# Kernel tuning notes

Measured on AMD Instinct MI355X. Metric: run time of the kernel, lower is better.

The kernel has to match this reference:

```python
import jax, jax.numpy as jnp
import numpy as np

EPS = 1e-15


def gmm_conv(x, edge_index, edge_attr, g, mu, sigma, root_w, bias):
    # PyG GMMConv (separate_gaussians=False, aggr='mean', root_weight=True)
    N = x.shape[0]
    K, D = mu.shape          # kernel_size, pseudo-coord dim
    M = bias.shape[0]        # out channels
    src, dst = edge_index[0], edge_index[1]
    xg = (x @ g).reshape(N, K, M)            # [N, K, M] transformed source feats
    x_j = xg[src]                            # [E, K, M] gather
    diff = edge_attr[:, None, :] - mu[None]  # [E, K, D]
    gauss = jnp.exp(jnp.sum(-0.5 * diff * diff / (EPS + sigma[None] ** 2), axis=-1))  # [E, K]
    msg = jnp.sum(x_j * gauss[:, :, None], axis=1)          # [E, M]
    agg = jax.ops.segment_sum(msg, dst, num_segments=N)     # scatter-sum
    cnt = jax.ops.segment_sum(jnp.ones((msg.shape[0], 1), msg.dtype), dst, num_segments=N)
    out = agg / jnp.maximum(cnt, 1.0)                        # scatter-mean (0 for isolated nodes)
    return out + x @ root_w + bias


def setup_inputs() -> dict:
    key = jax.random.key(0)
    ks = jax.random.split(key, 16)
    N, E, D, K = 100000, 1600000, 8, 1
    F_in, H, F_out = 32, 32, 32
    inp = {
        "edge_index": jax.random.randint(ks[0], (2, E), 0, N, dtype=jnp.int64)
        if jax.config.jax_enable_x64 else jax.random.randint(ks[0], (2, E), 0, N).astype(jnp.int32),
        "edge_weight": jax.random.normal(ks[1], (E, D), dtype=jnp.float32),
        "x": jax.random.normal(ks[2], (N, F_in), dtype=jnp.float32),
        # layer 1 params
        "g1": jax.random.normal(ks[3], (F_in, K * H), dtype=jnp.float32) * (1.0 / np.sqrt(F_in)),
        "mu1": jax.random.normal(ks[4], (K, D), dtype=jnp.float32),
        "sigma1": jnp.ones((K, D), dtype=jnp.float32),
        "root1": jax.random.normal(ks[5], (F_in, H), dtype=jnp.float32) * (1.0 / np.sqrt(F_in)),
        "b1": jnp.zeros((H,), dtype=jnp.float32),
        # layer 2 params
        "g2": jax.random.normal(ks[6], (H, K * F_out), dtype=jnp.float32) * (1.0 / np.sqrt(H)),
        "mu2": jax.random.normal(ks[7], (K, D), dtype=jnp.float32),
        "sigma2": jnp.ones((K, D), dtype=jnp.float32),
        "root2": jax.random.normal(ks[8], (H, F_out), dtype=jnp.float32) * (1.0 / np.sqrt(H)),
        "b2": jnp.zeros((F_out,), dtype=jnp.float32),
    }
    return inp


def reference(edge_index, edge_weight, x, g1, mu1, sigma1, root1, b1, g2, mu2, sigma2, root2, b2):
    h = gmm_conv(x, edge_index, edge_weight, g1, mu1, sigma1, root1, b1)
    out = gmm_conv(h, edge_index, edge_weight, g2, mu2, sigma2, root2, b2)
    return out
```

## Files before the change

### kernel.cpp

```cpp
#include <hip/hip_runtime.h>

#define F 32
#define D 8
#define BKN 512
#define BKSH 9
#define EPT 8
#define CAP 9216

typedef unsigned uv2 __attribute__((ext_vector_type(2)));
typedef float fv2 __attribute__((ext_vector_type(2)));
typedef float fv4 __attribute__((ext_vector_type(4)));

__device__ __forceinline__ unsigned f2bf(float f) {
    unsigned u = __float_as_uint(f);
    return (u + 0x7fffu + ((u >> 16) & 1u)) >> 16;
}
__device__ __forceinline__ float bf2f(unsigned b) {
    return __uint_as_float(b << 16);
}

__global__ void build_kernel(const int* __restrict__ ei, const float* __restrict__ ew,
                             const float* __restrict__ mu1, const float* __restrict__ sg1,
                             const float* __restrict__ mu2, const float* __restrict__ sg2,
                             int* __restrict__ bcur, uv2* __restrict__ bin, int NB, int E,
                             const float* __restrict__ x, const float* __restrict__ g1,
                             const float* __restrict__ root1, const float* __restrict__ b1,
                             unsigned short* __restrict__ xgh, float* __restrict__ xr,
                             int N, int binBlocks) {
    __shared__ int hist[512];
    __shared__ int cbase[512];
    __shared__ float gs[F * F];
    __shared__ float rs[F * F];
    int t = threadIdx.x;

    if ((int)blockIdx.x < binBlocks) {
        float m1v[D], i1[D], m2v[D], i2[D];
#pragma unroll
        for (int d = 0; d < D; ++d) {
            m1v[d] = mu1[d];
            i1[d] = -0.5f / (1e-15f + sg1[d] * sg1[d]);
            m2v[d] = mu2[d];
            i2[d] = -0.5f / (1e-15f + sg2[d] * sg2[d]);
        }
        if (t < NB) hist[t] = 0;
        __syncthreads();
        int e0 = blockIdx.x * (512 * EPT) + t;
        unsigned pks[EPT], gps[EPT];
        int bks[EPT];
#pragma unroll
        for (int k = 0; k < EPT; ++k) {
            int e = e0 + k * 512;
            bks[k] = -1;
            if (e < E) {
                int src = __builtin_nontemporal_load(&ei[e]);
                int dst = __builtin_nontemporal_load(&ei[E + e]);
                bks[k] = dst >> BKSH;
                pks[k] = (unsigned)src | ((unsigned)(dst & (BKN - 1)) << 20);
                const fv4* ew4 = (const fv4*)(ew + (size_t)e * D);
                fv4 w0 = __builtin_nontemporal_load(ew4);
                fv4 w1 = __builtin_nontemporal_load(ew4 + 1);
                float w[D] = {w0.x, w0.y, w0.z, w0.w, w1.x, w1.y, w1.z, w1.w};
                float s1 = 0.f, s2 = 0.f;
#pragma unroll
                for (int d = 0; d < D; ++d) {
                    float d1 = w[d] - m1v[d];
                    s1 += d1 * d1 * i1[d];
                    float d2 = w[d] - m2v[d];
                    s2 += d2 * d2 * i2[d];
                }
                gps[k] = f2bf(expf(s1)) | (f2bf(expf(s2)) << 16);
                atomicAdd(&hist[bks[k]], 1);
            }
        }
        __syncthreads();
        if (t < NB) {
            int c = hist[t];
            cbase[t] = t * CAP + (c ? atomicAdd(&bcur[t], c) : 0);
        }
        __syncthreads();
        if (t < NB) hist[t] = 0;
        __syncthreads();
#pragma unroll
        for (int k = 0; k < EPT; ++k) {
            if (bks[k] >= 0) {
                int pos = cbase[bks[k]] + atomicAdd(&hist[bks[k]], 1);
                if (pos < (bks[k] + 1) * CAP) {
                    uv2 p;
                    p.x = pks[k];
                    p.y = gps[k];
                    bin[pos] = p;
                }
            }
        }
    } else {
        for (int i = t; i < F * F; i += 512) {
            gs[i] = g1[i];
            rs[i] = root1[i];
        }
        __syncthreads();
        int m = t & 31;
        int node = (int)((((size_t)blockIdx.x - binBlocks) * 512 + t) >> 5);
        if (node >= N) return;
        float xv = x[(size_t)node * F + m];
        int base = t & 32;
        float accg = 0.f, accr = 0.f;
#pragma unroll
        for (int c = 0; c < F; ++c) {
            float xc = __shfl(xv, base + c, 64);
            accg += xc * gs[c * F + m];
            accr += xc * rs[c * F + m];
        }
        xgh[(size_t)node * F + m] = (unsigned short)f2bf(accg);
        xr[(size_t)node * F + m] = accr + b1[m];
    }
}

__global__ void csr_kernel(const uv2* __restrict__ bin, const int* __restrict__ bcur,
                           int2* __restrict__ off2, uv2* __restrict__ edata, int N) {
    int b = blockIdx.x;
    int ebase = b * CAP;
    int nE = min(bcur[b], CAP);
    __shared__ int cnt[BKN];
    __shared__ int cur[BKN];
    __shared__ int ps[BKN];
    int t = threadIdx.x;
    if (t < BKN) cnt[t] = 0;
    __syncthreads();
    for (int i = t; i < nE; i += 1024)
        atomicAdd(&cnt[(bin[ebase + i].x >> 20) & (BKN - 1)], 1);
    __syncthreads();
    int a = (t < BKN) ? cnt[t] : 0;
    if (t < BKN) ps[t] = a;
    __syncthreads();
    for (int d = 1; d < BKN; d <<= 1) {
        int u = (t < BKN && t >= d) ? ps[t - d] : 0;
        __syncthreads();
        if (t < BKN) ps[t] += u;
        __syncthreads();
    }
    if (t < BKN) {
        int excl = ps[t] - a;
        cur[t] = excl;
        int node = (b << BKSH) + t;
        if (node < N) {
            int2 o;
            o.x = ebase + excl;
            o.y = ebase + excl + a;
            off2[node] = o;
        }
    }
    __syncthreads();
    for (int i = t; i < nE; i += 1024) {
        uv2 p = bin[ebase + i];
        int dl = (p.x >> 20) & (BKN - 1);
        int pos = ebase + atomicAdd(&cur[dl], 1);
        uv2 q;
        q.x = p.x & 0xfffffu;
        q.y = p.y;
        edata[pos] = q;
    }
}

__global__ void agg1_fuse_kernel(const int2* __restrict__ off2,
                                 const uv2* __restrict__ edata,
                                 const unsigned* __restrict__ xg32,
                                 const fv2* __restrict__ xr2,
                                 const float* __restrict__ g2,
                                 const float* __restrict__ root2,
                                 const float* __restrict__ b2,
                                 unsigned* __restrict__ xg32_out,
                                 float2* __restrict__ xr2_out,
                                 int N) {
    __shared__ float gs[F * F];
    __shared__ float rs[F * F];
    for (int i = threadIdx.x; i < F * F; i += blockDim.x) {
        gs[i] = g2[i];
        rs[i] = root2[i];
    }
    __syncthreads();
    int t = threadIdx.x;
    int l = t & 15;
    int node = (int)((blockIdx.x * (size_t)blockDim.x + t) >> 4);
    if (node >= N) return;
    int base = t & 48;
    int2 so = off2[node];
    int s0 = so.x, s1 = so.y;
    int deg = s1 - s0;
    float a0 = 0.f, a1 = 0.f;
    for (int i = s0; i < s1; i += 16) {
        unsigned pk = 0;
        float gv = 0.f;
        if (i + l < s1) {
            uv2 ed = __builtin_nontemporal_load(&edata[i + l]);
            pk = ed.x;
            gv = bf2f(ed.y & 0xffffu);
        }
#pragma unroll
        for (int j = 0; j < 16; ++j) {
            if (i + j < s1) {
                unsigned s = __shfl(pk, base + j, 64);
                float g = __shfl(gv, base + j, 64);
                unsigned xv = xg32[s * 16 + l];
                a0 += bf2f(xv & 0xffffu) * g;
                a1 += __uint_as_float(xv & 0xffff0000u) * g;
            }
        }
    }
    float inv = (deg > 0) ? 1.f / (float)deg : 0.f;
    fv2 r = __builtin_nontemporal_load(&xr2[(size_t)node * 16 + l]);
    float hx = a0 * inv + r.x;
    float hy = a1 * inv + r.y;
    float ag0 = 0.f, ag1 = 0.f, ar0 = 0.f, ar1 = 0.f;
#pragma unroll
    for (int c = 0; c < F; ++c) {
        float src = (c & 1) ? hy : hx;
        float hc = __shfl(src, base + (c >> 1), 64);
        ag0 += hc * gs[c * F + 2 * l];
        ag1 += hc * gs[c * F + 2 * l + 1];
        ar0 += hc * rs[c * F + 2 * l];
        ar1 += hc * rs[c * F + 2 * l + 1];
    }
    xg32_out[(size_t)node * 16 + l] = f2bf(ag0) | (f2bf(ag1) << 16);
    float2 xo;
    xo.x = ar0 + b2[2 * l];
    xo.y = ar1 + b2[2 * l + 1];
    xr2_out[(size_t)node * 16 + l] = xo;
}

__global__ void aggregate2_kernel(const int2* __restrict__ off2,
                                  const uv2* __restrict__ edata,
                                  const unsigned* __restrict__ xg32,
                                  const fv2* __restrict__ xr2,
                                  fv2* __restrict__ out2, int N) {
    int t = threadIdx.x;
    int l = t & 15;
    int node = (int)((blockIdx.x * (size_t)blockDim.x + t) >> 4);
    if (node >= N) return;
    int base = t & 48;
    int2 so = off2[node];
    int s0 = so.x, s1 = so.y;
    int deg = s1 - s0;
    float a0 = 0.f, a1 = 0.f;
    for (int i = s0; i < s1; i += 16) {
        unsigned pk = 0;
        float gv = 0.f;
        if (i + l < s1) {
            uv2 ed = __builtin_nontemporal_load(&edata[i + l]);
            pk = ed.x;
            gv = __uint_as_float(ed.y & 0xffff0000u);
        }
#pragma unroll
        for (int j = 0; j < 16; ++j) {
            if (i + j < s1) {
                unsigned s = __shfl(pk, base + j, 64);
                float g = __shfl(gv, base + j, 64);
                unsigned xv = xg32[s * 16 + l];
                a0 += bf2f(xv & 0xffffu) * g;
                a1 += __uint_as_float(xv & 0xffff0000u) * g;
            }
        }
    }
    float inv = (deg > 0) ? 1.f / (float)deg : 0.f;
    fv2 r = __builtin_nontemporal_load(&xr2[(size_t)node * 16 + l]);
    fv2 o;
    o.x = a0 * inv + r.x;
    o.y = a1 * inv + r.y;
    __builtin_nontemporal_store(o, &out2[(size_t)node * 16 + l]);
}

extern "C" void kernel_launch(void* const* d_in, const int* in_sizes, int n_in,
                              void* d_out, int out_size, void* d_ws, size_t ws_size,
                              hipStream_t stream) {
    const int*   ei   = (const int*)d_in[0];
    const float* ew   = (const float*)d_in[1];
    const float* x    = (const float*)d_in[2];
    const float* g1   = (const float*)d_in[3];
    const float* mu1  = (const float*)d_in[4];
    const float* sg1  = (const float*)d_in[5];
    const float* r1   = (const float*)d_in[6];
    const float* b1   = (const float*)d_in[7];
    const float* g2   = (const float*)d_in[8];
    const float* mu2  = (const float*)d_in[9];
    const float* sg2  = (const float*)d_in[10];
    const float* r2   = (const float*)d_in[11];
    const float* b2   = (const float*)d_in[12];
    float* out = (float*)d_out;

    const int E = in_sizes[0] / 2;
    const int N = in_sizes[2] / F;
    const size_t NF = (size_t)N * F;
    const int NB = (N + BKN - 1) / BKN;

    uv2*            bin   = (uv2*)d_ws;
    uv2*            edata = bin + (size_t)NB * CAP;
    float*          xr1   = (float*)(edata + (size_t)NB * CAP);
    float*          xr2w  = xr1 + NF;
    unsigned short* xgh1  = (unsigned short*)(xr2w + NF);
    unsigned short* xgh2  = xgh1 + NF;
    int2*           off2  = (int2*)(xgh2 + NF);
    int*            bcur  = (int*)(off2 + N);

    const int BT = 256;
    const int blk_bin = (E + 512 * EPT - 1) / (512 * EPT);
    const int blk_tr  = (int)((NF + 511) / 512);
    const int blk_agg = (int)(((size_t)N * 16 + BT - 1) / BT);

    (void)hipMemsetAsync(bcur, 0, NB * sizeof(int), stream);

    build_kernel<<<blk_bin + blk_tr, 512, 0, stream>>>(
        ei, ew, mu1, sg1, mu2, sg2, bcur, bin, NB, E,
        x, g1, r1, b1, xgh1, xr1, N, blk_bin);

    csr_kernel<<<NB, 1024, 0, stream>>>(bin, bcur, off2, edata, N);

    agg1_fuse_kernel<<<blk_agg, BT, 0, stream>>>(off2, edata, (const unsigned*)xgh1,
                                                 (const fv2*)xr1, g2, r2, b2,
                                                 (unsigned*)xgh2, (float2*)xr2w, N);

    aggregate2_kernel<<<blk_agg, BT, 0, stream>>>(off2, edata, (const unsigned*)xgh2,
                                                  (const fv2*)xr2w, (fv2*)out, N);
}
```

Baseline: 266.1 us.

## Replace CSR build with per-bucket shared-memory atomic aggregation

Drops the CSR sort kernel. Each aggregation kernel now processes one destination bucket of 256 nodes per block and accumulates messages with shared-memory float atomics, reading the binned edges directly. The bucket size and capacity are halved so the accumulators fit in LDS. Layer 1 also stores the inverse degree for reuse in layer 2. This removes one kernel and the edata write and read traffic, at the cost of heavy LDS atomic contention and a non-deterministic summation order.

Measured after the change: 863.8 us. +224.6%, slower.

```diff
diff --git a/kernel.cpp b/kernel.cpp
--- a/kernel.cpp
+++ b/kernel.cpp
@@ -2,10 +2,10 @@
 
 #define F 32
 #define D 8
-#define BKN 512
-#define BKSH 9
+#define BKN 256
+#define BKSH 8
 #define EPT 8
-#define CAP 9216
+#define CAP 4608
 
 typedef unsigned uv2 __attribute__((ext_vector_type(2)));
 typedef float fv2 __attribute__((ext_vector_type(2)));
@@ -115,157 +115,164 @@
     }
 }
 
-__global__ void csr_kernel(const uv2* __restrict__ bin, const int* __restrict__ bcur,
-                           int2* __restrict__ off2, uv2* __restrict__ edata, int N) {
+__global__ __launch_bounds__(1024, 2) void agg1_bucket(
+        const uv2* __restrict__ bin, const int* __restrict__ bcur,
+        const uv2* __restrict__ xg64,
+        const float* __restrict__ xr1,
+        const float* __restrict__ g2, const float* __restrict__ root2,
+        const float* __restrict__ b2,
+        unsigned* __restrict__ xg32_out, float2* __restrict__ xr2_out,
+        float* __restrict__ invdeg, int N) {
+    __shared__ __align__(16) float acc[BKN * 33];
+    __shared__ int cnt[BKN];
+    __shared__ float invs[BKN];
+    __shared__ __align__(16) float gs[F * F];
+    __shared__ __align__(16) float rs[F * F];
+    int t = threadIdx.x;
     int b = blockIdx.x;
+    for (int i = t; i < BKN * 33; i += 1024) acc[i] = 0.f;
+    if (t < BKN) cnt[t] = 0;
+    for (int i = t; i < F * F; i += 1024) {
+        gs[i] = g2[i];
+        rs[i] = root2[i];
+    }
+    __syncthreads();
     int ebase = b * CAP;
     int nE = min(bcur[b], CAP);
-    __shared__ int cnt[BKN];
-    __shared__ int cur[BKN];
-    __shared__ int ps[BKN];
+    int l = t & 7;
+    int g = t >> 3;
+    for (int e = g; e < nE; e += 256) {
+        int e2 = e + 128;
+        bool hb = e2 < nE;
+        uv2 pa = bin[ebase + e];
+        uv2 pb;
+        pb.x = 0; pb.y = 0;
+        if (hb) pb = bin[ebase + e2];
+        unsigned sa = pa.x & 0xfffffu;
+        int dla = (pa.x >> 20) & (BKN - 1);
+        float ga = bf2f(pa.y & 0xffffu);
+        uv2 xa = xg64[(size_t)sa * 8 + l];
+        unsigned sb = pb.x & 0xfffffu;
+        int dlb = (pb.x >> 20) & (BKN - 1);
+        float gb = bf2f(pb.y & 0xffffu);
+        uv2 xb;
+        xb.x = 0; xb.y = 0;
+        if (hb) xb = xg64[(size_t)sb * 8 + l];
+        float* aa = &acc[dla * 33 + 4 * l];
+        atomicAdd(aa + 0, bf2f(xa.x & 0xffffu) * ga);
+        atomicAdd(aa + 1, __uint_as_float(xa.x & 0xffff0000u) * ga);
+        atomicAdd(aa + 2, bf2f(xa.y & 0xffffu) * ga);
+        atomicAdd(aa + 3, __uint_as_float(xa.y & 0xffff0000u) * ga);
+        if (l == 0) atomicAdd(&cnt[dla], 1);
+        if (hb) {
+            float* ab = &acc[dlb * 33 + 4 * l];
+            atomicAdd(ab + 0, bf2f(xb.x & 0xffffu) * gb);
+            atomicAdd(ab + 1, __uint_as_float(xb.x & 0xffff0000u) * gb);
+            atomicAdd(ab + 2, bf2f(xb.y & 0xffffu) * gb);
+            atomicAdd(ab + 3, __uint_as_float(xb.y & 0xffff0000u) * gb);
+            if (l == 0) atomicAdd(&cnt[dlb], 1);
+        }
+    }
+    __syncthreads();
+    int node0 = b << BKSH;
+    if (t < BKN) {
+        int c = cnt[t];
+        float inv = c > 0 ? 1.f / (float)c : 0.f;
+        invs[t] = inv;
+        if (node0 + t < N) invdeg[node0 + t] = inv;
+    }
+    __syncthreads();
+    for (int idx = t; idx < BKN * F; idx += 1024) {
+        int n = idx >> 5, c = idx & 31;
+        if (node0 + n < N)
+            acc[n * 33 + c] = acc[n * 33 + c] * invs[n] +
+                              __builtin_nontemporal_load(&xr1[(size_t)(node0 + n) * F + c]);
+    }
+    __syncthreads();
+    int ll = t & 15;
+    int grp = t >> 4;
+    fv2 b2v = ((const fv2*)b2)[ll];
+    for (int n = grp; n < BKN; n += 64) {
+        int node = node0 + n;
+        if (node >= N) continue;
+        const float* hrow = &acc[n * 33];
+        float ag0 = 0.f, ag1 = 0.f, ar0 = 0.f, ar1 = 0.f;
+#pragma unroll
+        for (int c = 0; c < F; ++c) {
+            float hc = hrow[c];
+            fv2 gv2 = ((const fv2*)gs)[c * 16 + ll];
+            fv2 rv2 = ((const fv2*)rs)[c * 16 + ll];
+            ag0 += hc * gv2.x;
+            ag1 += hc * gv2.y;
+            ar0 += hc * rv2.x;
+            ar1 += hc * rv2.y;
+        }
+        xg32_out[(size_t)node * 16 + ll] = f2bf(ag0) | (f2bf(ag1) << 16);
+        float2 xo;
+        xo.x = ar0 + b2v.x;
+        xo.y = ar1 + b2v.y;
+        xr2_out[(size_t)node * 16 + ll] = xo;
+    }
+}
+
+__global__ __launch_bounds__(1024, 2) void agg2_bucket(
+        const uv2* __restrict__ bin, const int* __restrict__ bcur,
+        const uv2* __restrict__ xg64,
+        const float* __restrict__ xr2,
+        const float* __restrict__ invdeg,
+        float* __restrict__ out, int N) {
+    __shared__ __align__(16) float acc[BKN * 33];
+    __shared__ float invs[BKN];
     int t = threadIdx.x;
-    if (t < BKN) cnt[t] = 0;
-    __syncthreads();
-    for (int i = t; i < nE; i += 1024)
-        atomicAdd(&cnt[(bin[ebase + i].x >> 20) & (BKN - 1)], 1);
-    __syncthreads();
-    int a = (t < BKN) ? cnt[t] : 0;
-    if (t < BKN) ps[t] = a;
-    __syncthreads();
-    for (int d = 1; d < BKN; d <<= 1) {
-        int u = (t < BKN && t >= d) ? ps[t - d] : 0;
-        __syncthreads();
-        if (t < BKN) ps[t] += u;
-        __syncthreads();
-    }
-    if (t < BKN) {
-        int excl = ps[t] - a;
-        cur[t] = excl;
-        int node = (b << BKSH) + t;
+    int b = blockIdx.x;
+    int node0 = b << BKSH;
+    for (int i = t; i < BKN * 33; i += 1024) acc[i] = 0.f;
+    if (t < BKN) invs[t] = (node0 + t < N) ? invdeg[node0 + t] : 0.f;
+    __syncthreads();
+    int ebase = b * CAP;
+    int nE = min(bcur[b], CAP);
+    int l = t & 7;
+    int g = t >> 3;
+    for (int e = g; e < nE; e += 256) {
+        int e2 = e + 128;
+        bool hb = e2 < nE;
+        uv2 pa = __builtin_nontemporal_load(&bin[ebase + e]);
+        uv2 pb;
+        pb.x = 0; pb.y = 0;
+        if (hb) pb = __builtin_nontemporal_load(&bin[ebase + e2]);
+        unsigned sa = pa.x & 0xfffffu;
+        int dla = (pa.x >> 20) & (BKN - 1);
+        float ga = __uint_as_float(pa.y & 0xffff0000u);
+        uv2 xa = xg64[(size_t)sa * 8 + l];
+        unsigned sb = pb.x & 0xfffffu;
+        int dlb = (pb.x >> 20) & (BKN - 1);
+        float gb = __uint_as_float(pb.y & 0xffff0000u);
+        uv2 xb;
+        xb.x = 0; xb.y = 0;
+        if (hb) xb = xg64[(size_t)sb * 8 + l];
+        float* aa = &acc[dla * 33 + 4 * l];
+        atomicAdd(aa + 0, bf2f(xa.x & 0xffffu) * ga);
+        atomicAdd(aa + 1, __uint_as_float(xa.x & 0xffff0000u) * ga);
+        atomicAdd(aa + 2, bf2f(xa.y & 0xffffu) * ga);
+        atomicAdd(aa + 3, __uint_as_float(xa.y & 0xffff0000u) * ga);
+        if (hb) {
+            float* ab = &acc[dlb * 33 + 4 * l];
+            atomicAdd(ab + 0, bf2f(xb.x & 0xffffu) * gb);
+            atomicAdd(ab + 1, __uint_as_float(xb.x & 0xffff0000u) * gb);
+            atomicAdd(ab + 2, bf2f(xb.y & 0xffffu) * gb);
+            atomicAdd(ab + 3, __uint_as_float(xb.y & 0xffff0000u) * gb);
+        }
+    }
+    __syncthreads();
+    for (int idx = t; idx < BKN * F; idx += 1024) {
+        int n = idx >> 5, c = idx & 31;
+        int node = node0 + n;
         if (node < N) {
-            int2 o;
-            o.x = ebase + excl;
-            o.y = ebase + excl + a;
-            off2[node] = o;
-        }
-    }
-    __syncthreads();
-    for (int i = t; i < nE; i += 1024) {
-        uv2 p = bin[ebase + i];
-        int dl = (p.x >> 20) & (BKN - 1);
-        int pos = ebase + atomicAdd(&cur[dl], 1);
-        uv2 q;
-        q.x = p.x & 0xfffffu;
-        q.y = p.y;
-        edata[pos] = q;
-    }
-}
-
-__global__ void agg1_fuse_kernel(const int2* __restrict__ off2,
-                                 const uv2* __restrict__ edata,
-                                 const unsigned* __restrict__ xg32,
-                                 const fv2* __restrict__ xr2,
-                                 const float* __restrict__ g2,
-                                 const float* __restrict__ root2,
-                                 const float* __restrict__ b2,
-                                 unsigned* __restrict__ xg32_out,
-                                 float2* __restrict__ xr2_out,
-                                 int N) {
-    __shared__ float gs[F * F];
-    __shared__ float rs[F * F];
-    for (int i = threadIdx.x; i < F * F; i += blockDim.x) {
-        gs[i] = g2[i];
-        rs[i] = root2[i];
-    }
-    __syncthreads();
-    int t = threadIdx.x;
-    int l = t & 15;
-    int node = (int)((blockIdx.x * (size_t)blockDim.x + t) >> 4);
-    if (node >= N) return;
-    int base = t & 48;
-    int2 so = off2[node];
-    int s0 = so.x, s1 = so.y;
-    int deg = s1 - s0;
-    float a0 = 0.f, a1 = 0.f;
-    for (int i = s0; i < s1; i += 16) {
-        unsigned pk = 0;
-        float gv = 0.f;
-        if (i + l < s1) {
-            uv2 ed = __builtin_nontemporal_load(&edata[i + l]);
-            pk = ed.x;
-            gv = bf2f(ed.y & 0xffffu);
-        }
-#pragma unroll
-        for (int j = 0; j < 16; ++j) {
-            if (i + j < s1) {
-                unsigned s = __shfl(pk, base + j, 64);
-                float g = __shfl(gv, base + j, 64);
-                unsigned xv = xg32[s * 16 + l];
-                a0 += bf2f(xv & 0xffffu) * g;
-                a1 += __uint_as_float(xv & 0xffff0000u) * g;
-            }
-        }
-    }
-    float inv = (deg > 0) ? 1.f / (float)deg : 0.f;
-    fv2 r = __builtin_nontemporal_load(&xr2[(size_t)node * 16 + l]);
-    float hx = a0 * inv + r.x;
-    float hy = a1 * inv + r.y;
-    float ag0 = 0.f, ag1 = 0.f, ar0 = 0.f, ar1 = 0.f;
-#pragma unroll
-    for (int c = 0; c < F; ++c) {
-        float src = (c & 1) ? hy : hx;
-        float hc = __shfl(src, base + (c >> 1), 64);
-        ag0 += hc * gs[c * F + 2 * l];
-        ag1 += hc * gs[c * F + 2 * l + 1];
-        ar0 += hc * rs[c * F + 2 * l];
-        ar1 += hc * rs[c * F + 2 * l + 1];
-    }
-    xg32_out[(size_t)node * 16 + l] = f2bf(ag0) | (f2bf(ag1) << 16);
-    float2 xo;
-    xo.x = ar0 + b2[2 * l];
-    xo.y = ar1 + b2[2 * l + 1];
-    xr2_out[(size_t)node * 16 + l] = xo;
-}
-
-__global__ void aggregate2_kernel(const int2* __restrict__ off2,
-                                  const uv2* __restrict__ edata,
-                                  const unsigned* __restrict__ xg32,
-                                  const fv2* __restrict__ xr2,
-                                  fv2* __restrict__ out2, int N) {
-    int t = threadIdx.x;
-    int l = t & 15;
-    int node = (int)((blockIdx.x * (size_t)blockDim.x + t) >> 4);
-    if (node >= N) return;
-    int base = t & 48;
-    int2 so = off2[node];
-    int s0 = so.x, s1 = so.y;
-    int deg = s1 - s0;
-    float a0 = 0.f, a1 = 0.f;
-    for (int i = s0; i < s1; i += 16) {
-        unsigned pk = 0;
-        float gv = 0.f;
-        if (i + l < s1) {
-            uv2 ed = __builtin_nontemporal_load(&edata[i + l]);
-            pk = ed.x;
-            gv = __uint_as_float(ed.y & 0xffff0000u);
-        }
-#pragma unroll
-        for (int j = 0; j < 16; ++j) {
-            if (i + j < s1) {
-                unsigned s = __shfl(pk, base + j, 64);
-                float g = __shfl(gv, base + j, 64);
-                unsigned xv = xg32[s * 16 + l];
-                a0 += bf2f(xv & 0xffffu) * g;
-                a1 += __uint_as_float(xv & 0xffff0000u) * g;
-            }
-        }
-    }
-    float inv = (deg > 0) ? 1.f / (float)deg : 0.f;
-    fv2 r = __builtin_nontemporal_load(&xr2[(size_t)node * 16 + l]);
-    fv2 o;
-    o.x = a0 * inv + r.x;
-    o.y = a1 * inv + r.y;
-    __builtin_nontemporal_store(o, &out2[(size_t)node * 16 + l]);
+            float v = acc[n * 33 + c] * invs[n] +
+                      __builtin_nontemporal_load(&xr2[(size_t)node * F + c]);
+            __builtin_nontemporal_store(v, &out[(size_t)node * F + c]);
+        }
+    }
 }
 
 extern "C" void kernel_launch(void* const* d_in, const int* in_sizes, int n_in,
@@ -291,19 +298,16 @@
     const size_t NF = (size_t)N * F;
     const int NB = (N + BKN - 1) / BKN;
 
-    uv2*            bin   = (uv2*)d_ws;
-    uv2*            edata = bin + (size_t)NB * CAP;
-    float*          xr1   = (float*)(edata + (size_t)NB * CAP);
-    float*          xr2w  = xr1 + NF;
-    unsigned short* xgh1  = (unsigned short*)(xr2w + NF);
-    unsigned short* xgh2  = xgh1 + NF;
-    int2*           off2  = (int2*)(xgh2 + NF);
-    int*            bcur  = (int*)(off2 + N);
-
-    const int BT = 256;
+    uv2*            bin    = (uv2*)d_ws;
+    float*          xr1    = (float*)(bin + (size_t)NB * CAP);
+    float*          xr2w   = xr1 + NF;
+    unsigned short* xgh1   = (unsigned short*)(xr2w + NF);
+    unsigned short* xgh2   = xgh1 + NF;
+    float*          invdeg = (float*)(xgh2 + NF);
+    int*            bcur   = (int*)(invdeg + N);
+
     const int blk_bin = (E + 512 * EPT - 1) / (512 * EPT);
     const int blk_tr  = (int)((NF + 511) / 512);
-    const int blk_agg = (int)(((size_t)N * 16 + BT - 1) / BT);
 
     (void)hipMemsetAsync(bcur, 0, NB * sizeof(int), stream);
 
@@ -311,12 +315,10 @@
         ei, ew, mu1, sg1, mu2, sg2, bcur, bin, NB, E,
         x, g1, r1, b1, xgh1, xr1, N, blk_bin);
 
-    csr_kernel<<<NB, 1024, 0, stream>>>(bin, bcur, off2, edata, N);
-
-    agg1_fuse_kernel<<<blk_agg, BT, 0, stream>>>(off2, edata, (const unsigned*)xgh1,
-                                                 (const fv2*)xr1, g2, r2, b2,
-                                                 (unsigned*)xgh2, (float2*)xr2w, N);
-
-    aggregate2_kernel<<<blk_agg, BT, 0, stream>>>(off2, edata, (const unsigned*)xgh2,
-                                                  (const fv2*)xr2w, (fv2*)out, N);
-}
+    agg1_bucket<<<NB, 1024, 0, stream>>>(bin, bcur, (const uv2*)xgh1, xr1,
+                                         g2, r2, b2,
+                                         (unsigned*)xgh2, (float2*)xr2w, invdeg, N);
+
+    agg2_bucket<<<NB, 1024, 0, stream>>>(bin, bcur, (const uv2*)xgh2, xr2w,
+                                         invdeg, out, N);
+}
```
